# Performance work log

Hardware: AMD Instinct MI355X
Metric: run time of the kernel (lower is better)

## Reference

```python
import jax, jax.numpy as jnp
import numpy as np

C, H, N, B, L = 1, 512, 64, 16, 2048  # n_channels, n_heads, d_kernel, batch, seq_len


def setup_inputs() -> dict:
    key = jax.random.key(0)
    k1, k2 = jax.random.split(key)
    u = jax.random.normal(k1, (B, C * H, L), dtype=jnp.float32)
    k = jax.random.normal(k2, (C, H, N), dtype=jnp.float32)
    return {"u": u, "k": k}


def _l1_normalize(x, axis):
    # torch.linalg.norm(x, ord=1, dim=axis, keepdim=True): vector 1-norm along `axis`
    return x / jnp.sum(jnp.abs(x), axis=axis, keepdims=True)


def _forward(u, k):
    c, h, n = k.shape
    bsz, d, l = u.shape  # d == c*h
    dt = u.dtype
    # Shift matrix A: A[:, :, 1:, :-1] = I  (companion-style shift)
    A = jnp.zeros((c, h, n, n), dtype=dt).at[:, :, 1:, :-1].set(jnp.eye(n - 1, dtype=dt))
    # b = e1 broadcast to (c, h, n)
    b_vec = jnp.zeros((c, h, n), dtype=dt).at[:, :, 0].set(1.0)
    # closed-loop: k_norm = L1-normalize(clamp(k, 1/16, 1)); A_cl = L1-normalize(A + b k^T)
    k_norm = _l1_normalize(jnp.clip(k, 1.0 / 16.0, 1.0), axis=2)
    BK = jnp.einsum('chi,chj->chij', b_vec, k_norm)
    M = _l1_normalize(A + BK, axis=2)

    # Krylov recurrence: f[i] = k . (M^i b), i = 0..l-1
    def step(x, _):
        f_i = jnp.einsum('chn,chn->ch', k, x)
        x_next = jnp.einsum('chij,chj->chi', M, x)
        return x_next, f_i

    _, f = jax.lax.scan(step, b_vec, None, length=l)  # f: (l, c, h)
    f = jnp.moveaxis(f, 0, -1)  # (c, h, l)

    # Causal FFT convolution of u (b, c, h, l) with filter f (c, h, l)
    n_fft = 2 * l
    uf = jnp.fft.rfft(u.reshape(bsz, c, h, l), n=n_fft)
    ff = jnp.fft.rfft(f, n=n_fft)
    y = jnp.fft.irfft(uf * ff[None], n=n_fft)[..., :l]
    return y.reshape(bsz, c * h, l)


def reference(u, k):
    return _forward(u, k)
```

## Files before the change

kernel.cpp:

```cpp
#include <hip/hip_runtime.h>


namespace {

constexpr int kH = 512;
constexpr int kL = 2048;
constexpr int kChunks = 32;
constexpr int kStride = 68;

typedef __attribute__((ext_vector_type(8))) short bf16x8;
typedef __attribute__((ext_vector_type(4))) float f32x4;

#define MFMA(A, B, C) __builtin_amdgcn_mfma_f32_16x16x32_bf16((A), (B), (C), 0, 0, 0)

__device__ inline unsigned int cvt_pk_bf16(float lo, float hi) {
  unsigned int r;
  asm("v_cvt_pk_bf16_f32 %0, %1, %2" : "=v"(r) : "v"(lo), "v"(hi));
  return r;
}

union B8U4 { bf16x8 v; unsigned int u[4]; };

__device__ inline void cvt_split8(const f32x4 a, const f32x4 b, bf16x8& fh, bf16x8& fl) {
  B8U4 H, L;
  float x[8];
  #pragma unroll
  for (int j = 0; j < 4; ++j) { x[j] = a[j]; x[4 + j] = b[j]; }
  #pragma unroll
  for (int d = 0; d < 4; ++d) {
    const float x0 = x[2 * d], x1 = x[2 * d + 1];
    const unsigned int hp = cvt_pk_bf16(x0, x1);
    const float h0 = __uint_as_float(hp << 16);
    const float h1 = __uint_as_float(hp & 0xFFFF0000u);
    H.u[d] = hp;
    L.u[d] = cvt_pk_bf16(x0 - h0, x1 - h1);
  }
  fh = H.v; fl = L.v;
}

__device__ inline void gen_frag(const float* tp, int n0, bf16x8& fh, bf16x8& fl) {
  float t[8];
  #pragma unroll
  for (int j = 0; j < 8; ++j) {
    const int n = n0 - j;
    t[j] = (n >= 0 && n < 127) ? tp[n] : 0.0f;
  }
  const f32x4 a = {t[0], t[1], t[2], t[3]};
  const f32x4 b = {t[4], t[5], t[6], t[7]};
  cvt_split8(a, b, fh, fl);
}

__global__ __launch_bounds__(256, 2)
void ssm_mfma_kernel(const float* __restrict__ u,
                     const float* __restrict__ kin,
                     float* __restrict__ y) {
  const int h    = blockIdx.x;
  const int tid  = threadIdx.x;
  const int wq   = tid >> 6;
  const int lane = tid & 63;
  const int ln16 = lane & 15;
  const int quad = lane >> 4;

  __shared__ float sArr[64], gArr[64], wPad[128];
  __shared__ float taps[3][128];
  __shared__ float Abuf[64][kStride];
  __shared__ float Rbuf[2][16][kStride];

  if (wq == 0) {
    const float kv = kin[h * 64 + lane];
    const float kc = fminf(fmaxf(kv, 0.0625f), 1.0f);
    float ks = kc;
    #pragma unroll
    for (int off = 32; off >= 1; off >>= 1) ks += __shfl_xor(ks, off);
    const float kn = kc / ks;
    const float cc = 1.0f / (1.0f + kn);
    float pp = cc;
    #pragma unroll
    for (int off = 1; off < 64; off <<= 1) {
      const float t = __shfl_up(pp, off);
      if (lane >= off) pp *= t;
    }
    float Pe = __shfl_up(pp, 1);
    if (lane == 0) Pe = 1.0f;
    const float w = (lane < 63) ? (kn * cc * Pe) : Pe;
    const float g = kv * Pe;
    float s = (lane == 0) ? 1.0f : 0.0f;
    for (int rr = 0; rr < 63; ++rr) {
      const float sv = __shfl(s, rr);
      const float cf = __shfl(w, lane - 1 - rr);
      if (lane > rr) s = fmaf(cf, sv, s);
    }
    sArr[lane] = s;
    gArr[lane] = g;
    wPad[lane] = w;
    wPad[lane + 64] = 0.0f;
  }
  __syncthreads();

  for (int idx = tid; idx < 384; idx += 256) {
    const int c = idx >> 7, n = idx & 127;
    float v;
    if (c == 0)      v = (n >= 63 && n < 127) ? sArr[n - 63] : 0.0f;
    else if (c == 1) v = (n >= 63 && n < 127) ? gArr[n - 63] : 0.0f;
    else             v = (n < 63) ? gArr[n + 1] : 0.0f;
    taps[c][n] = v;
  }
  __syncthreads();

  bf16x8 sH[2], sL[2], g2H[2], g2L[2], g1H[2], g1L[2], aH[2], aL[2];
  #pragma unroll
  for (int tk = 0; tk < 2; ++tk) {
    const int n0 = 16 * wq + ln16 - (32 * tk + 8 * quad) + 63;
    gen_frag(taps[0], n0, sH[tk], sL[tk]);
    gen_frag(taps[1], n0, g2H[tk], g2L[tk]);
    gen_frag(taps[2], n0, g1H[tk], g1L[tk]);
  }

  {
    f32x4 accA[4];
    #pragma unroll
    for (int nt = 0; nt < 4; ++nt) accA[nt] = (f32x4){0.f, 0.f, 0.f, 0.f};
    #pragma unroll
    for (int nt = 0; nt < 4; ++nt) {
      #pragma unroll
      for (int tk = 0; tk < 2; ++tk) {
        float t[8];
        #pragma unroll
        for (int j = 0; j < 8; ++j)
          t[j] = wPad[(8 * quad + 32 * tk + j) - (16 * nt + ln16) + 63];
        const f32x4 a = {t[0], t[1], t[2], t[3]};
        const f32x4 b = {t[4], t[5], t[6], t[7]};
        bf16x8 wh, wl;
        cvt_split8(a, b, wh, wl);
        accA[nt] = MFMA(sH[tk], wh, accA[nt]);
        accA[nt] = MFMA(sH[tk], wl, accA[nt]);
        accA[nt] = MFMA(sL[tk], wh, accA[nt]);
        accA[nt] = MFMA(sL[tk], wl, accA[nt]);
      }
    }
    #pragma unroll
    for (int nt = 0; nt < 4; ++nt) {
      #pragma unroll
      for (int r = 0; r < 4; ++r)
        Abuf[16 * wq + 4 * quad + r][16 * nt + ln16] = accA[nt][r];
    }
  }
  __syncthreads();
  #pragma unroll
  for (int tk = 0; tk < 2; ++tk) {
    const int row = 16 * wq + ln16;
    const int k0 = 32 * tk + 8 * quad;
    const f32x4 a = *(const f32x4*)&Abuf[row][k0];
    const f32x4 b = *(const f32x4*)&Abuf[row][k0 + 4];
    cvt_split8(a, b, aH[tk], aL[tk]);
  }

  bf16x8 pH[2], pL[2];
  {
    bf16x8 z;
    #pragma unroll
    for (int j = 0; j < 8; ++j) z[j] = 0;
    pH[0] = z; pH[1] = z; pL[0] = z; pL[1] = z;
  }

  const float* ub = u + ((size_t)ln16 * kH + h) * kL + 8 * quad;
  float* yp = y + ((size_t)ln16 * kH + h) * kL + 16 * wq + 4 * quad;
  const int ewrow = 16 * wq + 4 * quad;

  f32x4 uv[4];
  #pragma unroll
  for (int i = 0; i < 4; ++i)
    uv[i] = *(const f32x4*)(ub + 32 * (i >> 1) + 4 * (i & 1));

  int buf = 0;
  for (int m = 0; m < kChunks; ++m) {
    const int t0 = m * 64;
    bf16x8 uH[2], uL[2];
    cvt_split8(uv[0], uv[1], uH[0], uL[0]);
    cvt_split8(uv[2], uv[3], uH[1], uL[1]);
    const int tn = (m < kChunks - 1) ? t0 + 64 : t0;
    #pragma unroll
    for (int i = 0; i < 4; ++i)
      uv[i] = *(const f32x4*)(ub + tn + 32 * (i >> 1) + 4 * (i & 1));

    f32x4 accP = {};
    #pragma unroll
    for (int tk = 0; tk < 2; ++tk) {
      accP = MFMA(aH[tk], pH[tk], accP);
      accP = MFMA(aH[tk], pL[tk], accP);
      accP = MFMA(aL[tk], pH[tk], accP);
    }
    f32x4 accU = {};
    #pragma unroll
    for (int tk = 0; tk < 2; ++tk) {
      accU = MFMA(sH[tk], uH[tk], accU);
      accU = MFMA(sH[tk], uL[tk], accU);
      accU = MFMA(sL[tk], uH[tk], accU);
    }
    f32x4 accY = {};
    #pragma unroll
    for (int tk = 0; tk < 2; ++tk) {
      accY = MFMA(g1H[tk], pH[tk], accY);
      accY = MFMA(g1H[tk], pL[tk], accY);
      accY = MFMA(g1L[tk], pH[tk], accY);
    }
    const f32x4 accR = accP + accU;
    *(f32x4*)&Rbuf[buf][ln16][ewrow] = accR;
    asm volatile("s_waitcnt lgkmcnt(0)" ::: "memory");
    __builtin_amdgcn_s_barrier();
    asm volatile("" ::: "memory");

    #pragma unroll
    for (int tk = 0; tk < 2; ++tk) {
      const int k0 = 8 * quad + 32 * tk;
      const f32x4 ra = *(const f32x4*)&Rbuf[buf][ln16][k0];
      const f32x4 rb = *(const f32x4*)&Rbuf[buf][ln16][k0 + 4];
      cvt_split8(ra, rb, pH[tk], pL[tk]);
    }
    f32x4 accY2 = accY;
    #pragma unroll
    for (int tk = 0; tk < 2; ++tk) {
      accY2 = MFMA(g2H[tk], pH[tk], accY2);
      accY2 = MFMA(g2H[tk], pL[tk], accY2);
      accY2 = MFMA(g2L[tk], pH[tk], accY2);
    }
    *(f32x4*)(yp + t0) = accY2;
    buf ^= 1;
  }
}

}

extern "C" void kernel_launch(void* const* d_in, const int* in_sizes, int n_in,
                              void* d_out, int out_size, void* d_ws, size_t ws_size,
                              hipStream_t stream) {
  const float* u  = (const float*)d_in[0];
  const float* kk = (const float*)d_in[1];
  if (n_in >= 2 && in_sizes[0] < in_sizes[1]) {
    const float* t = u; u = kk; kk = t;
  }
  float* y = (float*)d_out;
  hipLaunchKernelGGL(ssm_mfma_kernel, dim3(kH), dim3(256), 0, stream, u, kk, y);
}
```

Measured before the change: 154.7 us.

## Collapse each head's block to a single wavefront to remove per-chunk barriers

Each head now runs on one 64-lane wavefront instead of four waves. That wave handles all four 16-row M tiles in the chunked scan, so the per-chunk s_barrier between waves goes away and Rbuf no longer needs double buffering. The g1/g2 fragments move to LDS to limit register pressure, and the u prefetch is double-buffered two chunks ahead. In exchange each wave issues four times the MFMAs serially, and occupancy is only 512 single-wave blocks across the device, so less latency hiding is available.

```diff
diff --git a/kernel.cpp b/kernel.cpp
--- a/kernel.cpp
+++ b/kernel.cpp
@@ -50,76 +50,75 @@
   cvt_split8(a, b, fh, fl);
 }
 
-__global__ __launch_bounds__(256, 2)
+__global__ __launch_bounds__(64, 1)
 void ssm_mfma_kernel(const float* __restrict__ u,
                      const float* __restrict__ kin,
                      float* __restrict__ y) {
   const int h    = blockIdx.x;
-  const int tid  = threadIdx.x;
-  const int wq   = tid >> 6;
-  const int lane = tid & 63;
+  const int lane = threadIdx.x;
   const int ln16 = lane & 15;
   const int quad = lane >> 4;
 
-  __shared__ float sArr[64], gArr[64], wPad[128];
   __shared__ float taps[3][128];
+  __shared__ float wPad[128];
   __shared__ float Abuf[64][kStride];
-  __shared__ float Rbuf[2][16][kStride];
-
-  if (wq == 0) {
-    const float kv = kin[h * 64 + lane];
-    const float kc = fminf(fmaxf(kv, 0.0625f), 1.0f);
-    float ks = kc;
-    #pragma unroll
-    for (int off = 32; off >= 1; off >>= 1) ks += __shfl_xor(ks, off);
-    const float kn = kc / ks;
-    const float cc = 1.0f / (1.0f + kn);
-    float pp = cc;
-    #pragma unroll
-    for (int off = 1; off < 64; off <<= 1) {
-      const float t = __shfl_up(pp, off);
-      if (lane >= off) pp *= t;
-    }
-    float Pe = __shfl_up(pp, 1);
-    if (lane == 0) Pe = 1.0f;
-    const float w = (lane < 63) ? (kn * cc * Pe) : Pe;
-    const float g = kv * Pe;
-    float s = (lane == 0) ? 1.0f : 0.0f;
-    for (int rr = 0; rr < 63; ++rr) {
-      const float sv = __shfl(s, rr);
-      const float cf = __shfl(w, lane - 1 - rr);
-      if (lane > rr) s = fmaf(cf, sv, s);
-    }
-    sArr[lane] = s;
-    gArr[lane] = g;
-    wPad[lane] = w;
-    wPad[lane + 64] = 0.0f;
-  }
+  __shared__ float Rbuf[16][kStride];
+  __shared__ bf16x8 g2T[4][2][2][64];
+  __shared__ bf16x8 g1T[4][2][2][64];
+
+  const float kv = kin[h * 64 + lane];
+  const float kc = fminf(fmaxf(kv, 0.0625f), 1.0f);
+  float ks = kc;
+  #pragma unroll
+  for (int off = 32; off >= 1; off >>= 1) ks += __shfl_xor(ks, off);
+  const float kn = kc / ks;
+  const float cc = 1.0f / (1.0f + kn);
+  float pp = cc;
+  #pragma unroll
+  for (int off = 1; off < 64; off <<= 1) {
+    const float t = __shfl_up(pp, off);
+    if (lane >= off) pp *= t;
+  }
+  float Pe = __shfl_up(pp, 1);
+  if (lane == 0) Pe = 1.0f;
+  const float w = (lane < 63) ? (kn * cc * Pe) : Pe;
+  const float g = kv * Pe;
+  float s = (lane == 0) ? 1.0f : 0.0f;
+  for (int rr = 0; rr < 63; ++rr) {
+    const float sv = __shfl(s, rr);
+    const float cf = __shfl(w, lane - 1 - rr);
+    if (lane > rr) s = fmaf(cf, sv, s);
+  }
+  taps[0][lane] = 0.0f;
+  taps[1][lane] = 0.0f;
+  const float gn = __shfl(g, lane + 1);
+  taps[2][lane] = (lane < 63) ? gn : 0.0f;
+  taps[2][64 + lane] = 0.0f;
+  taps[0][63 + lane] = s;
+  taps[1][63 + lane] = g;
+  wPad[lane] = w;
+  wPad[64 + lane] = 0.0f;
   __syncthreads();
 
-  for (int idx = tid; idx < 384; idx += 256) {
-    const int c = idx >> 7, n = idx & 127;
-    float v;
-    if (c == 0)      v = (n >= 63 && n < 127) ? sArr[n - 63] : 0.0f;
-    else if (c == 1) v = (n >= 63 && n < 127) ? gArr[n - 63] : 0.0f;
-    else             v = (n < 63) ? gArr[n + 1] : 0.0f;
-    taps[c][n] = v;
-  }
-  __syncthreads();
-
-  bf16x8 sH[2], sL[2], g2H[2], g2L[2], g1H[2], g1L[2], aH[2], aL[2];
-  #pragma unroll
-  for (int tk = 0; tk < 2; ++tk) {
-    const int n0 = 16 * wq + ln16 - (32 * tk + 8 * quad) + 63;
-    gen_frag(taps[0], n0, sH[tk], sL[tk]);
-    gen_frag(taps[1], n0, g2H[tk], g2L[tk]);
-    gen_frag(taps[2], n0, g1H[tk], g1L[tk]);
+  bf16x8 sH[4][2], sL[4][2], aH[4][2], aL[4][2];
+  #pragma unroll
+  for (int mt = 0; mt < 4; ++mt) {
+    #pragma unroll
+    for (int tk = 0; tk < 2; ++tk) {
+      const int n0 = 16 * mt + ln16 - (32 * tk + 8 * quad) + 63;
+      gen_frag(taps[0], n0, sH[mt][tk], sL[mt][tk]);
+      bf16x8 fh, fl;
+      gen_frag(taps[1], n0, fh, fl);
+      g2T[mt][tk][0][lane] = fh;
+      g2T[mt][tk][1][lane] = fl;
+      gen_frag(taps[2], n0, fh, fl);
+      g1T[mt][tk][0][lane] = fh;
+      g1T[mt][tk][1][lane] = fl;
+    }
   }
 
   {
-    f32x4 accA[4];
-    #pragma unroll
-    for (int nt = 0; nt < 4; ++nt) accA[nt] = (f32x4){0.f, 0.f, 0.f, 0.f};
+    bf16x8 wh[4][2], wl[4][2];
     #pragma unroll
     for (int nt = 0; nt < 4; ++nt) {
       #pragma unroll
@@ -130,29 +129,43 @@
           t[j] = wPad[(8 * quad + 32 * tk + j) - (16 * nt + ln16) + 63];
         const f32x4 a = {t[0], t[1], t[2], t[3]};
         const f32x4 b = {t[4], t[5], t[6], t[7]};
-        bf16x8 wh, wl;
-        cvt_split8(a, b, wh, wl);
-        accA[nt] = MFMA(sH[tk], wh, accA[nt]);
-        accA[nt] = MFMA(sH[tk], wl, accA[nt]);
-        accA[nt] = MFMA(sL[tk], wh, accA[nt]);
-        accA[nt] = MFMA(sL[tk], wl, accA[nt]);
-      }
-    }
-    #pragma unroll
-    for (int nt = 0; nt < 4; ++nt) {
-      #pragma unroll
-      for (int r = 0; r < 4; ++r)
-        Abuf[16 * wq + 4 * quad + r][16 * nt + ln16] = accA[nt][r];
+        cvt_split8(a, b, wh[nt][tk], wl[nt][tk]);
+      }
+    }
+    #pragma unroll
+    for (int mt = 0; mt < 4; ++mt) {
+      f32x4 accA[4];
+      #pragma unroll
+      for (int nt = 0; nt < 4; ++nt) accA[nt] = (f32x4){0.f, 0.f, 0.f, 0.f};
+      #pragma unroll
+      for (int nt = 0; nt < 4; ++nt) {
+        #pragma unroll
+        for (int tk = 0; tk < 2; ++tk) {
+          accA[nt] = MFMA(sH[mt][tk], wh[nt][tk], accA[nt]);
+          accA[nt] = MFMA(sH[mt][tk], wl[nt][tk], accA[nt]);
+          accA[nt] = MFMA(sL[mt][tk], wh[nt][tk], accA[nt]);
+          accA[nt] = MFMA(sL[mt][tk], wl[nt][tk], accA[nt]);
+        }
+      }
+      #pragma unroll
+      for (int nt = 0; nt < 4; ++nt) {
+        #pragma unroll
+        for (int r = 0; r < 4; ++r)
+          Abuf[16 * mt + 4 * quad + r][16 * nt + ln16] = accA[nt][r];
+      }
     }
   }
   __syncthreads();
   #pragma unroll
-  for (int tk = 0; tk < 2; ++tk) {
-    const int row = 16 * wq + ln16;
-    const int k0 = 32 * tk + 8 * quad;
-    const f32x4 a = *(const f32x4*)&Abuf[row][k0];
-    const f32x4 b = *(const f32x4*)&Abuf[row][k0 + 4];
-    cvt_split8(a, b, aH[tk], aL[tk]);
+  for (int mt = 0; mt < 4; ++mt) {
+    #pragma unroll
+    for (int tk = 0; tk < 2; ++tk) {
+      const int row = 16 * mt + ln16;
+      const int k0 = 32 * tk + 8 * quad;
+      const f32x4 a = *(const f32x4*)&Abuf[row][k0];
+      const f32x4 b = *(const f32x4*)&Abuf[row][k0 + 4];
+      cvt_split8(a, b, aH[mt][tk], aL[mt][tk]);
+    }
   }
 
   bf16x8 pH[2], pL[2];
@@ -164,68 +177,87 @@
   }
 
   const float* ub = u + ((size_t)ln16 * kH + h) * kL + 8 * quad;
-  float* yp = y + ((size_t)ln16 * kH + h) * kL + 16 * wq + 4 * quad;
-  const int ewrow = 16 * wq + 4 * quad;
-
-  f32x4 uv[4];
-  #pragma unroll
-  for (int i = 0; i < 4; ++i)
-    uv[i] = *(const f32x4*)(ub + 32 * (i >> 1) + 4 * (i & 1));
-
-  int buf = 0;
-  for (int m = 0; m < kChunks; ++m) {
-    const int t0 = m * 64;
+  float* yp = y + ((size_t)ln16 * kH + h) * kL + 4 * quad;
+
+  auto chunk = [&](f32x4 (&uvC)[4], int t0, int tpre) {
     bf16x8 uH[2], uL[2];
-    cvt_split8(uv[0], uv[1], uH[0], uL[0]);
-    cvt_split8(uv[2], uv[3], uH[1], uL[1]);
-    const int tn = (m < kChunks - 1) ? t0 + 64 : t0;
+    cvt_split8(uvC[0], uvC[1], uH[0], uL[0]);
+    cvt_split8(uvC[2], uvC[3], uH[1], uL[1]);
     #pragma unroll
     for (int i = 0; i < 4; ++i)
-      uv[i] = *(const f32x4*)(ub + tn + 32 * (i >> 1) + 4 * (i & 1));
-
-    f32x4 accP = {};
-    #pragma unroll
-    for (int tk = 0; tk < 2; ++tk) {
-      accP = MFMA(aH[tk], pH[tk], accP);
-      accP = MFMA(aH[tk], pL[tk], accP);
-      accP = MFMA(aL[tk], pH[tk], accP);
-    }
-    f32x4 accU = {};
-    #pragma unroll
-    for (int tk = 0; tk < 2; ++tk) {
-      accU = MFMA(sH[tk], uH[tk], accU);
-      accU = MFMA(sH[tk], uL[tk], accU);
-      accU = MFMA(sL[tk], uH[tk], accU);
-    }
-    f32x4 accY = {};
-    #pragma unroll
-    for (int tk = 0; tk < 2; ++tk) {
-      accY = MFMA(g1H[tk], pH[tk], accY);
-      accY = MFMA(g1H[tk], pL[tk], accY);
-      accY = MFMA(g1L[tk], pH[tk], accY);
-    }
-    const f32x4 accR = accP + accU;
-    *(f32x4*)&Rbuf[buf][ln16][ewrow] = accR;
+      uvC[i] = *(const f32x4*)(ub + tpre + 32 * (i >> 1) + 4 * (i & 1));
+
+    f32x4 accR[4], accY[4];
+    #pragma unroll
+    for (int mt = 0; mt < 4; ++mt) {
+      accR[mt] = (f32x4){0.f, 0.f, 0.f, 0.f};
+      accY[mt] = (f32x4){0.f, 0.f, 0.f, 0.f};
+    }
+    #pragma unroll
+    for (int mt = 0; mt < 4; ++mt) {
+      #pragma unroll
+      for (int tk = 0; tk < 2; ++tk) {
+        accR[mt] = MFMA(aH[mt][tk], pH[tk], accR[mt]);
+        accR[mt] = MFMA(aH[mt][tk], pL[tk], accR[mt]);
+        accR[mt] = MFMA(aL[mt][tk], pH[tk], accR[mt]);
+      }
+      #pragma unroll
+      for (int tk = 0; tk < 2; ++tk) {
+        accR[mt] = MFMA(sH[mt][tk], uH[tk], accR[mt]);
+        accR[mt] = MFMA(sH[mt][tk], uL[tk], accR[mt]);
+        accR[mt] = MFMA(sL[mt][tk], uH[tk], accR[mt]);
+      }
+    }
+    #pragma unroll
+    for (int mt = 0; mt < 4; ++mt)
+      *(f32x4*)&Rbuf[ln16][16 * mt + 4 * quad] = accR[mt];
+
+    #pragma unroll
+    for (int mt = 0; mt < 4; ++mt) {
+      #pragma unroll
+      for (int tk = 0; tk < 2; ++tk) {
+        const bf16x8 gh = g1T[mt][tk][0][lane];
+        const bf16x8 gl = g1T[mt][tk][1][lane];
+        accY[mt] = MFMA(gh, pH[tk], accY[mt]);
+        accY[mt] = MFMA(gh, pL[tk], accY[mt]);
+        accY[mt] = MFMA(gl, pH[tk], accY[mt]);
+      }
+    }
+
     asm volatile("s_waitcnt lgkmcnt(0)" ::: "memory");
-    __builtin_amdgcn_s_barrier();
-    asm volatile("" ::: "memory");
-
+    __builtin_amdgcn_sched_barrier(0);
     #pragma unroll
     for (int tk = 0; tk < 2; ++tk) {
       const int k0 = 8 * quad + 32 * tk;
-      const f32x4 ra = *(const f32x4*)&Rbuf[buf][ln16][k0];
-      const f32x4 rb = *(const f32x4*)&Rbuf[buf][ln16][k0 + 4];
+      const f32x4 ra = *(const f32x4*)&Rbuf[ln16][k0];
+      const f32x4 rb = *(const f32x4*)&Rbuf[ln16][k0 + 4];
       cvt_split8(ra, rb, pH[tk], pL[tk]);
     }
-    f32x4 accY2 = accY;
-    #pragma unroll
-    for (int tk = 0; tk < 2; ++tk) {
-      accY2 = MFMA(g2H[tk], pH[tk], accY2);
-      accY2 = MFMA(g2H[tk], pL[tk], accY2);
-      accY2 = MFMA(g2L[tk], pH[tk], accY2);
-    }
-    *(f32x4*)(yp + t0) = accY2;
-    buf ^= 1;
+
+    #pragma unroll
+    for (int mt = 0; mt < 4; ++mt) {
+      #pragma unroll
+      for (int tk = 0; tk < 2; ++tk) {
+        const bf16x8 gh = g2T[mt][tk][0][lane];
+        const bf16x8 gl = g2T[mt][tk][1][lane];
+        accY[mt] = MFMA(gh, pH[tk], accY[mt]);
+        accY[mt] = MFMA(gh, pL[tk], accY[mt]);
+        accY[mt] = MFMA(gl, pH[tk], accY[mt]);
+      }
+      *(f32x4*)(yp + t0 + 16 * mt) = accY[mt];
+    }
+  };
+
+  f32x4 uvA[4], uvB[4];
+  #pragma unroll
+  for (int i = 0; i < 4; ++i) {
+    uvA[i] = *(const f32x4*)(ub + 32 * (i >> 1) + 4 * (i & 1));
+    uvB[i] = *(const f32x4*)(ub + 64 + 32 * (i >> 1) + 4 * (i & 1));
+  }
+  for (int m = 0; m < kChunks; m += 2) {
+    const int t0 = m * 64;
+    chunk(uvA, t0,      (t0 + 128 < kL) ? (t0 + 128) : 0);
+    chunk(uvB, t0 + 64, (t0 + 192 < kL) ? (t0 + 192) : 0);
   }
 }
 
@@ -240,5 +272,5 @@
     const float* t = u; u = kk; kk = t;
   }
   float* y = (float*)d_out;
-  hipLaunchKernelGGL(ssm_mfma_kernel, dim3(kH), dim3(256), 0, stream, u, kk, y);
-}
+  hipLaunchKernelGGL(ssm_mfma_kernel, dim3(kH), dim3(64), 0, stream, u, kk, y);
+}
```

Measured after the change: 145.9 us. 5.7% less time.
